# Performance work log

Measured on AMD Instinct MI355X. Metric: run time of the kernel, lower is better.

The kernel has to match this reference:

```python
import jax, jax.numpy as jnp
import numpy as np
import math

B, S, D, H = 4, 1024, 1024, 16
HD = D // H  # 64
DFF = 4 * D
LN_EPS = 1e-5

def setup_inputs() -> dict:
    key = jax.random.key(0)
    ks = jax.random.split(key, 24)
    sd = lambda fi, fo: 1.0 / math.sqrt(fi)
    def lin(k, fi, fo):
        k1, k2 = jax.random.split(k)
        w = jax.random.uniform(k1, (fi, fo), jnp.float32, -sd(fi, fo), sd(fi, fo))
        b = jax.random.uniform(k2, (fo,), jnp.float32, -sd(fi, fo), sd(fi, fo))
        return w, b
    x = jax.random.normal(ks[0], (B, S, D), jnp.float32)
    Wk, bk = lin(ks[1], D, D)
    Wq, bq = lin(ks[2], D, D)
    Wv, bv = lin(ks[3], D, D)
    # per-head projections stacked over heads: [H, D, HD]
    def head_lin(k):
        kk = jax.random.split(k, H)
        ws, bs = zip(*[lin(kk[h], D, HD) for h in range(H)])
        return jnp.stack(ws), jnp.stack(bs)
    Whq, bhq = head_lin(ks[4])
    Whk, bhk = head_lin(ks[5])
    Whv, bhv = head_lin(ks[6])
    Wo, bo = lin(ks[7], D, D)
    W1, b1 = lin(ks[8], D, DFF)
    W2, b2 = lin(ks[9], DFF, D)
    gamma = jnp.ones((D,), jnp.float32)
    beta = jnp.zeros((D,), jnp.float32)
    return dict(x=x, Wk=Wk, bk=bk, Wq=Wq, bq=bq, Wv=Wv, bv=bv,
                Whq=Whq, bhq=bhq, Whk=Whk, bhk=bhk, Whv=Whv, bhv=bhv,
                Wo=Wo, bo=bo, W1=W1, b1=b1, W2=W2, b2=b2,
                gamma=gamma, beta=beta)

def _layer_norm(x, gamma, beta):
    mu = jnp.mean(x, axis=-1, keepdims=True)
    var = jnp.mean(jnp.square(x - mu), axis=-1, keepdims=True)
    return (x - mu) * jax.lax.rsqrt(var + LN_EPS) * gamma + beta

def reference(x, Wk, bk, Wq, bq, Wv, bv, Whq, bhq, Whk, bhk, Whv, bhv,
              Wo, bo, W1, b1, W2, b2, gamma, beta):
    # outer projections; NOTE: forward passes (k, q, v) into MHA, so the
    # MHA 'Q' stream is k_proj(x), 'K' stream is q_proj(x), 'V' is v_proj(x)
    ko = x @ Wk + bk
    qo = x @ Wq + bq
    vo = x @ Wv + bv
    # per-head projections (batched over heads): [B,H,S,HD]
    q = jnp.einsum('bsd,hde->bhse', ko, Whq) + bhq[None, :, None, :]
    k = jnp.einsum('bsd,hde->bhse', qo, Whk) + bhk[None, :, None, :]
    v = jnp.einsum('bsd,hde->bhse', vo, Whv) + bhv[None, :, None, :]
    # NOTE: original scales by sqrt(d_model), not sqrt(head_dim)
    scores = jnp.einsum('bhse,bhte->bhst', q, k) / math.sqrt(D)
    w = jax.nn.softmax(scores, axis=-1)
    o = jnp.einsum('bhst,bhte->bhse', w, v)         # [B,H,S,HD]
    o = o.transpose(0, 2, 1, 3).reshape(B, S, D)    # concat heads
    attn = o @ Wo + bo
    # dropout is identity in eval; shared LayerNorm after both residuals
    r1 = _layer_norm(x + attn, gamma, beta)
    ff = jax.nn.gelu(r1 @ W1 + b1, approximate=False) @ W2 + b2
    out = _layer_norm(r1 + ff, gamma, beta)
    return out
```

## Files before the change

### kernel.cpp

```cpp
#include <hip/hip_runtime.h>
#include <cstdint>
#include <cstddef>

#define D_MODEL 1024
#define SEQ 1024
#define BATCH 4
#define NHEAD 16
#define HDIM 64
#define ROWS (BATCH*SEQ)

typedef unsigned short u16;
typedef __attribute__((ext_vector_type(4))) unsigned short u16x4;
typedef __attribute__((ext_vector_type(8))) unsigned short u16x8;
typedef __attribute__((ext_vector_type(8))) __bf16 bf16x8v;
typedef __attribute__((ext_vector_type(4))) float f32x4;

__device__ inline u16 f2bf(float f){
  union{float f; unsigned u;} c; c.f = f;
  unsigned r = c.u + 0x7FFFu + ((c.u>>16)&1u);
  return (u16)(r>>16);
}
__device__ inline float bf2f(u16 s){
  union{unsigned u; float f;} c; c.u = ((unsigned)s)<<16; return c.f;
}
__device__ inline float gelu_f(float x){ return 0.5f*x*(1.f+erff(x*0.7071067811865475f)); }

__device__ __forceinline__ void gload_lds16(const void* g, void* l){
  __builtin_amdgcn_global_load_lds(
    (const __attribute__((address_space(1))) unsigned int*)g,
    (__attribute__((address_space(3))) unsigned int*)l, 16, 0, 0);
}

__global__ __launch_bounds__(256) void convert_bf(const float* __restrict__ in, u16* __restrict__ out){
  size_t idx = (size_t)blockIdx.x*256 + threadIdx.x;
  f32x4 v = *(const f32x4*)(in + idx*4);
  u16x4 o = { f2bf(v.x), f2bf(v.y), f2bf(v.z), f2bf(v.w) };
  *(u16x4*)(out + idx*4) = o;
}

struct C3 { const float* src[3]; u16* dst[3]; };
__global__ __launch_bounds__(256) void convert_w3(C3 p){
  int z = blockIdx.z;
  size_t idx = (size_t)blockIdx.x*256 + threadIdx.x;
  f32x4 v = *(const f32x4*)(p.src[z] + idx*4);
  u16x4 o = { f2bf(v.x), f2bf(v.y), f2bf(v.z), f2bf(v.w) };
  *(u16x4*)(p.dst[z] + idx*4) = o;
}

__global__ __launch_bounds__(256) void transpose_conv(const float* __restrict__ W, u16* __restrict__ WT, int K, int N){
  __shared__ float tile[32][33];
  int n0 = blockIdx.x*32, k0 = blockIdx.y*32;
  int tx = threadIdx.x & 31, ty = threadIdx.x >> 5;
  #pragma unroll
  for (int i=0;i<4;i++){
    int r = ty + i*8;
    tile[r][tx] = W[(size_t)(k0+r)*N + n0 + tx];
  }
  __syncthreads();
  #pragma unroll
  for (int i=0;i<4;i++){
    int r = ty + i*8;
    WT[(size_t)(n0+r)*K + k0 + tx] = f2bf(tile[tx][r]);
  }
}

struct H3 { const float* src[3]; u16* dst[3]; };
__global__ __launch_bounds__(256) void head_transpose3(H3 p){
  __shared__ float tile[32][33];
  int z = blockIdx.z; int which = z >> 4; int h = z & 15;
  const float* Wh = p.src[which];
  u16* WT = p.dst[which];
  int d0 = blockIdx.x*32, e0 = blockIdx.y*32;
  int tx = threadIdx.x & 31, ty = threadIdx.x >> 5;
  #pragma unroll
  for (int i=0;i<4;i++){
    int r = ty + i*8;
    tile[r][tx] = Wh[(size_t)h*D_MODEL*HDIM + (size_t)(d0+r)*HDIM + e0 + tx];
  }
  __syncthreads();
  #pragma unroll
  for (int i=0;i<4;i++){
    int r = ty + i*8;
    WT[(size_t)(h*HDIM + e0 + r)*D_MODEL + d0 + tx] = f2bf(tile[tx][r]);
  }
}

__global__ __launch_bounds__(64) void bias_comb(
  const float* bk, const float* bq, const float* bv,
  const float* Whq, const float* Whk, const float* Whv,
  const float* bhq, const float* bhk, const float* bhv, float* bc)
{
  int blk = blockIdx.x; int which = blk >> 4; int h = blk & 15; int e = threadIdx.x;
  const float* bvec = (which==0) ? bk : (which==1) ? bq : bv;
  const float* Wh   = (which==0) ? Whq : (which==1) ? Whk : Whv;
  const float* bh   = (which==0) ? bhq : (which==1) ? bhk : bhv;
  float s = bh[h*HDIM + e];
  const float* w = Wh + (size_t)h*D_MODEL*HDIM + e;
  for (int d=0; d<D_MODEL; ++d) s += bvec[d] * w[(size_t)d*HDIM];
  bc[which*1024 + h*HDIM + e] = s;
}

__global__ __launch_bounds__(512,2) void gemm256_8p(
  const u16* __restrict__ A, const u16* __restrict__ BT, const float* __restrict__ bias,
  u16* __restrict__ outB, int N, int K, int mode, int act)
{
  __shared__ __align__(16) u16 As[2][2][128*64];
  __shared__ __align__(16) u16 Bs[2][2][128*64];
  int t = threadIdx.x, lane = t&63, wid = t>>6;
  int wr = wid>>2, wc = wid&3;
  int fr = lane&15, kg = lane>>4;
  int gx = gridDim.x;
  int bid = blockIdx.y*gx + blockIdx.x;
  int nwg = gx*gridDim.y;
  int cpx = nwg>>3;
  int sw = (bid&7)*cpx + (bid>>3);
  int tc = sw % gx, tr = sw / gx;

  const u16* Abase = A  + (size_t)tr*256*K;
  const u16* Bbase = BT + (size_t)tc*256*K;
  int srow = lane>>3, sch8 = lane&7;

  f32x4 acc[8][4];
  #pragma unroll
  for (int m=0;m<8;m++)
    #pragma unroll
    for (int n=0;n<4;n++) acc[m][n] = (f32x4)0.f;

  bf16x8v af[2][4], bv0[2][2], bv1[2][2];

  #define STAGE_A8(buf,h,kt) { _Pragma("unroll") for (int li=0;li<2;li++){ \
    int sr = (wid*2+li)*8 + srow; \
    int gr = ((sr>>6)<<7) + (h)*64 + (sr&63); \
    int sc = sch8 ^ (sr&7); \
    gload_lds16(Abase + (size_t)gr*K + (size_t)(kt)*64 + sc*8, &As[buf][h][(wid*2+li)*512]); } }
  #define STAGE_B8(buf,h,kt) { _Pragma("unroll") for (int li=0;li<2;li++){ \
    int sr = (wid*2+li)*8 + srow; \
    int gc = ((sr>>5)<<6) + (h)*32 + (sr&31); \
    int sc = sch8 ^ (sr&7); \
    gload_lds16(Bbase + (size_t)gc*K + (size_t)(kt)*64 + sc*8, &Bs[buf][h][(wid*2+li)*512]); } }
  #define LDA8(buf,h) { _Pragma("unroll") for (int ks=0;ks<2;ks++) _Pragma("unroll") for (int mf=0;mf<4;mf++){ \
    int r = wr*64 + mf*16 + fr; \
    af[ks][mf] = *(const bf16x8v*)&As[buf][h][r*64 + (((kg+4*ks)^(r&7)))*8]; } }
  #define LDB8(buf,h,dst) { _Pragma("unroll") for (int ks=0;ks<2;ks++) _Pragma("unroll") for (int nf=0;nf<2;nf++){ \
    int r = wc*32 + nf*16 + fr; \
    dst[ks][nf] = *(const bf16x8v*)&Bs[buf][h][r*64 + (((kg+4*ks)^(r&7)))*8]; } }
  #define MM8(mq,nq,bv) { asm volatile("s_waitcnt lgkmcnt(0)" ::: "memory"); \
    __builtin_amdgcn_s_setprio(1); \
    _Pragma("unroll") for (int ks=0;ks<2;ks++) _Pragma("unroll") for (int mf=0;mf<4;mf++) _Pragma("unroll") for (int nf=0;nf<2;nf++) \
      acc[(mq)*4+mf][(nq)*2+nf] = __builtin_amdgcn_mfma_f32_16x16x32_bf16(af[ks][mf], bv[ks][nf], acc[(mq)*4+mf][(nq)*2+nf], 0,0,0); \
    __builtin_amdgcn_s_setprio(0); }
  #define BAR asm volatile("s_barrier" ::: "memory")

  int NT = K >> 6;
  STAGE_A8(0,0,0); STAGE_B8(0,0,0); STAGE_B8(0,1,0); STAGE_A8(0,1,0);
  asm volatile("s_waitcnt vmcnt(4)" ::: "memory");
  BAR;

  for (int kt=0; kt<NT; ++kt){
    int buf = kt&1, nb = buf^1;
    int pre = (kt+1 < NT);
    LDA8(buf,0); LDB8(buf,0,bv0);
    if (pre){ STAGE_A8(nb,0,kt+1); asm volatile("s_waitcnt vmcnt(4)" ::: "memory"); }
    else    {                      asm volatile("s_waitcnt vmcnt(2)" ::: "memory"); }
    BAR; MM8(0,0,bv0); BAR;
    LDB8(buf,1,bv1);
    if (pre){ STAGE_B8(nb,0,kt+1); asm volatile("s_waitcnt vmcnt(4)" ::: "memory"); }
    else    {                      asm volatile("s_waitcnt vmcnt(0)" ::: "memory"); }
    BAR; MM8(0,1,bv1); BAR;
    LDA8(buf,1);
    if (pre){ STAGE_B8(nb,1,kt+1); asm volatile("s_waitcnt vmcnt(6)" ::: "memory"); }
    BAR; MM8(1,1,bv1); BAR;
    if (pre){ STAGE_A8(nb,1,kt+1); asm volatile("s_waitcnt vmcnt(4)" ::: "memory"); }
    BAR; MM8(1,0,bv0); BAR;
  }

  int crow0 = tr*256 + wr*128;
  int ccol0 = tc*256 + wc*64;
  #pragma unroll
  for (int n=0;n<4;n++){
    int col = ccol0 + n*16 + fr;
    float bv = bias[col];
    #pragma unroll
    for (int m=0;m<8;m++){
      int rbase = crow0 + m*16 + kg*4;
      #pragma unroll
      for (int i=0;i<4;i++){
        float v = acc[m][n][i] + bv;
        if (act) v = gelu_f(v);
        int row = rbase + i;
        if (mode == 1){
          outB[(size_t)row*N + col] = f2bf(v);
        } else {
          int panel = col >> 10, c1 = col & 1023;
          if (panel < 2)
            outB[(size_t)panel*((size_t)ROWS*1024) + (size_t)row*1024 + c1] = f2bf(v);
          else {
            int b = row >> 10, s = row & 1023;
            int hh = c1 >> 6, e = c1 & 63;
            outB[(size_t)2*((size_t)ROWS*1024) + (((size_t)((b*NHEAD+hh)*HDIM+e))<<10) + s] = f2bf(v);
          }
        }
      }
    }
  }
}

__device__ __forceinline__ void stage128(u16 (*As)[4096], u16 (*Bs)[4096], int b,
  const u16* Ab, const u16* Bb, int Kstride, int kt, int wid, int rr, int sch)
{
  #pragma unroll
  for (int c=0;c<2;c++){
    int reg = c*4 + wid;
    int row = reg*16 + rr;
    gload_lds16(Ab + (size_t)row*Kstride + kt*32 + sch*8, &As[b][reg*512]);
  }
  #pragma unroll
  for (int c=0;c<2;c++){
    int reg = c*4 + wid;
    int row = reg*16 + rr;
    gload_lds16(Bb + (size_t)row*Kstride + kt*32 + sch*8, &Bs[b][reg*512]);
  }
}

__device__ __forceinline__ void gemm128_core(u16 (*As)[4096], u16 (*Bs)[4096],
  const u16* __restrict__ A, const u16* __restrict__ BT, const float* __restrict__ bias,
  float* __restrict__ outF, u16* __restrict__ outB,
  int N, int Kstride, int kofs, int Ksub, int mode, int act, int addbias)
{
  int t = threadIdx.x, lane = t&63, wid = t>>6;
  int wr = wid>>1, wc = wid&1;
  int fr = lane&15, kg = lane>>4;
  int gx = gridDim.x;
  int bid = blockIdx.y*gx + blockIdx.x;
  int nwg = gx*gridDim.y;
  int cpx = nwg >> 3;
  int sw = (bid&7)*cpx + (bid>>3);
  int tc = sw % gx, tr = sw / gx;

  const u16* Ab = A  + (size_t)tr*128*Kstride + kofs;
  const u16* Bb = BT + (size_t)tc*128*Kstride + kofs;
  int rr = lane>>2, cc = lane&3;
  int sch = cc ^ ((rr>>1)&3);

  f32x4 acc[4][4];
  #pragma unroll
  for (int m=0;m<4;m++)
    #pragma unroll
    for (int n=0;n<4;n++) acc[m][n] = (f32x4)0.f;

  int NT = Ksub >> 5;

  stage128(As, Bs, 0, Ab, Bb, Kstride, 0, wid, rr, sch);
  stage128(As, Bs, 1, Ab, Bb, Kstride, 1, wid, rr, sch);
  int buf = 0;
  for (int kt=0; kt<NT; ++kt){
    if (kt+2 < NT){
      int nb = buf+2; if (nb>=3) nb-=3;
      stage128(As, Bs, nb, Ab, Bb, Kstride, kt+2, wid, rr, sch);
      asm volatile("s_waitcnt vmcnt(8)" ::: "memory");
    } else if (kt+1 < NT){
      asm volatile("s_waitcnt vmcnt(4)" ::: "memory");
    } else {
      asm volatile("s_waitcnt vmcnt(0)" ::: "memory");
    }
    asm volatile("s_barrier" ::: "memory");
    bf16x8v af[4], bfv[4];
    #pragma unroll
    for (int m=0;m<4;m++){
      int r = wr*64 + m*16 + fr;
      af[m] = *(const bf16x8v*)&As[buf][r*32 + (kg ^ ((r>>1)&3))*8];
    }
    #pragma unroll
    for (int n=0;n<4;n++){
      int r = wc*64 + n*16 + fr;
      bfv[n] = *(const bf16x8v*)&Bs[buf][r*32 + (kg ^ ((r>>1)&3))*8];
    }
    #pragma unroll
    for (int m=0;m<4;m++)
      #pragma unroll
      for (int n=0;n<4;n++)
        acc[m][n] = __builtin_amdgcn_mfma_f32_16x16x32_bf16(af[m], bfv[n], acc[m][n], 0,0,0);
    if (kt+1 < NT)
      asm volatile("s_barrier" ::: "memory");
    buf += 1; if (buf >= 3) buf = 0;
  }

  int crow0 = tr*128 + wr*64;
  int ccol0 = tc*128 + wc*64;
  #pragma unroll
  for (int n=0;n<4;n++){
    int col = ccol0 + n*16 + fr;
    float bv = addbias ? bias[col] : 0.f;
    #pragma unroll
    for (int m=0;m<4;m++){
      int rbase = crow0 + m*16 + kg*4;
      #pragma unroll
      for (int i=0;i<4;i++){
        float v = acc[m][n][i] + bv;
        if (act) v = gelu_f(v);
        int row = rbase + i;
        if (mode == 1){
          outB[(size_t)row*N + col] = f2bf(v);
        } else {
          outF[(size_t)row*1024 + col] = v;
        }
      }
    }
  }
}

__global__ __launch_bounds__(256) void g_gemm_sk(
  const u16* A, const u16* BT, const float* bias, float* outBase, int K)
{
  __shared__ __align__(16) u16 As[3][4096];
  __shared__ __align__(16) u16 Bs[3][4096];
  int z = blockIdx.z;
  int Ksub = K >> 1;
  gemm128_core(As, Bs, A, BT, bias, outBase + (size_t)z*ROWS*1024, nullptr,
               1024, K, z*Ksub, Ksub, 3, 0, z==0);
}

struct B3 { const u16* A[3]; const u16* BT[3]; u16* Cb[3]; };
__global__ __launch_bounds__(256) void g_gemm_b3(B3 p, const float* bias){
  __shared__ __align__(16) u16 As[3][4096];
  __shared__ __align__(16) u16 Bs[3][4096];
  int z = blockIdx.z;
  gemm128_core(As, Bs, p.A[z], p.BT[z], bias, nullptr, p.Cb[z],
               1024, 1024, 0, 1024, 1, 0, 0);
}

__global__ __launch_bounds__(256) void attn_mfma(const u16* __restrict__ Q, const u16* __restrict__ Km,
                                                 const u16* __restrict__ Vt, u16* __restrict__ O)
{
  __shared__ __align__(16) u16 Ks[2][64*64];
  __shared__ __align__(16) u16 Vs[2][64*64];
  __shared__ __align__(16) u16 Ps[4][16*64];
  int t = threadIdx.x, lane = t & 63, wid = t >> 6;
  int fr = lane & 15, kg = lane >> 4;
  int qt = blockIdx.x, h = blockIdx.y, b = blockIdx.z;
  const size_t qkbase = ((size_t)b*SEQ)*D_MODEL + (size_t)h*HDIM;
  const size_t vtb = ((size_t)(b*NHEAD + h))*HDIM*SEQ;

  int qrow = qt*64 + wid*16 + fr;
  bf16x8v aq0 = *(const bf16x8v*)(Q + qkbase + (size_t)qrow*D_MODEL + kg*8);
  bf16x8v aq1 = *(const bf16x8v*)(Q + qkbase + (size_t)qrow*D_MODEL + 32 + kg*8);

  f32x4 Oacc[4];
  #pragma unroll
  for (int n=0;n<4;n++) Oacc[n] = (f32x4)0.f;
  float m_run[4], l_run[4];
  #pragma unroll
  for (int i=0;i<4;i++){ m_run[i] = -3e38f; l_run[i] = 0.f; }

  int srow = lane >> 3;
  int sch  = (lane & 7) ^ srow;
  int x7 = fr & 7;
  const float CS = 0.03125f * 1.4426950408889634f;
  u16* Pw = &Ps[wid][0];

  #define ASTG(bf,kt) { _Pragma("unroll") for (int c=0;c<2;c++){ \
    int r0 = (wid*2 + c)*8; int rowk = r0 + srow; \
    gload_lds16(Km + qkbase + (size_t)((kt)*64 + rowk)*D_MODEL + sch*8, &Ks[bf][r0*64]); \
    gload_lds16(Vt + vtb + (size_t)rowk*SEQ + (kt)*64 + sch*8, &Vs[bf][r0*64]); } }

  ASTG(0,0);
  asm volatile("s_waitcnt vmcnt(0)" ::: "memory");
  __syncthreads();

  for (int kt = 0; kt < SEQ/64; ++kt){
    int bf = kt & 1;
    if (kt+1 < SEQ/64) ASTG(bf^1, kt+1);

    f32x4 s4[4];
    #pragma unroll
    for (int n=0;n<4;n++){
      int r = n*16 + fr;
      bf16x8v k0 = *(const bf16x8v*)&Ks[bf][r*64 + ((kg  ) ^ x7)*8];
      bf16x8v k1 = *(const bf16x8v*)&Ks[bf][r*64 + ((4+kg) ^ x7)*8];
      f32x4 z = (f32x4)0.f;
      z = __builtin_amdgcn_mfma_f32_16x16x32_bf16(aq0, k0, z, 0,0,0);
      s4[n] = __builtin_amdgcn_mfma_f32_16x16x32_bf16(aq1, k1, z, 0,0,0);
    }
    #pragma unroll
    for (int n=0;n<4;n++) s4[n] *= CS;

    float mI[4];
    #pragma unroll
    for (int i=0;i<4;i++)
      mI[i] = fmaxf(fmaxf(s4[0][i], s4[1][i]), fmaxf(s4[2][i], s4[3][i]));
    #pragma unroll
    for (int off=1; off<16; off<<=1){
      #pragma unroll
      for (int i=0;i<4;i++) mI[i] = fmaxf(mI[i], __shfl_xor(mI[i], off));
    }
    float g = -3e38f;
    #pragma unroll
    for (int i=0;i<4;i++) g = fmaxf(g, mI[i] - m_run[i]);
    if (__any(g > 8.f)){
      #pragma unroll
      for (int i=0;i<4;i++){
        float mn = fmaxf(m_run[i], mI[i]);
        float sc = exp2f(m_run[i] - mn);
        m_run[i] = mn;
        l_run[i] *= sc;
        #pragma unroll
        for (int n=0;n<4;n++) Oacc[n][i] *= sc;
      }
    }
    float ls[4] = {0.f,0.f,0.f,0.f};
    #pragma unroll
    for (int n=0;n<4;n++){
      int chunk = n*2 + (fr>>3);
      #pragma unroll
      for (int i=0;i<4;i++){
        float pv = exp2f(s4[n][i] - m_run[i]);
        ls[i] += pv;
        int row = kg*4 + i;
        Pw[row*64 + (chunk ^ (row&7))*8 + (fr&7)] = f2bf(pv);
      }
    }
    #pragma unroll
    for (int off=1; off<16; off<<=1){
      #pragma unroll
      for (int i=0;i<4;i++) ls[i] += __shfl_xor(ls[i], off);
    }
    #pragma unroll
    for (int i=0;i<4;i++) l_run[i] += ls[i];
    asm volatile("s_waitcnt lgkmcnt(0)" ::: "memory");

    bf16x8v ap0 = *(const bf16x8v*)&Pw[fr*64 + ((kg  ) ^ x7)*8];
    bf16x8v ap1 = *(const bf16x8v*)&Pw[fr*64 + ((4+kg) ^ x7)*8];
    #pragma unroll
    for (int n2=0;n2<4;n2++){
      int r = n2*16 + fr;
      bf16x8v v0 = *(const bf16x8v*)&Vs[bf][r*64 + ((kg  ) ^ x7)*8];
      bf16x8v v1 = *(const bf16x8v*)&Vs[bf][r*64 + ((4+kg) ^ x7)*8];
      Oacc[n2] = __builtin_amdgcn_mfma_f32_16x16x32_bf16(ap0, v0, Oacc[n2], 0,0,0);
      Oacc[n2] = __builtin_amdgcn_mfma_f32_16x16x32_bf16(ap1, v1, Oacc[n2], 0,0,0);
    }
    asm volatile("s_waitcnt vmcnt(0)" ::: "memory");
    __syncthreads();
  }

  float inv[4];
  #pragma unroll
  for (int i=0;i<4;i++) inv[i] = 1.f / l_run[i];
  #pragma unroll
  for (int n2=0;n2<4;n2++){
    #pragma unroll
    for (int i=0;i<4;i++){
      int row = qt*64 + wid*16 + kg*4 + i;
      O[qkbase + (size_t)row*D_MODEL + n2*16 + fr] = f2bf(Oacc[n2][i]*inv[i]);
    }
  }
}

__global__ __launch_bounds__(256) void ln_sum3(const float* __restrict__ A, const float* __restrict__ B,
   const float* __restrict__ C, const float* __restrict__ gamma, const float* __restrict__ beta,
   float* __restrict__ Of, u16* __restrict__ Ob)
{
  int row = blockIdx.x, t = threadIdx.x;
  size_t base = (size_t)row*D_MODEL + t*4;
  f32x4 v = *(const f32x4*)(A + base);
  v += *(const f32x4*)(B + base);
  v += *(const f32x4*)(C + base);
  float s = v.x+v.y+v.z+v.w;
  float q = v.x*v.x+v.y*v.y+v.z*v.z+v.w*v.w;
  #pragma unroll
  for (int off=1; off<64; off<<=1){ s += __shfl_xor(s,off); q += __shfl_xor(q,off); }
  __shared__ float red[8];
  int wid = t>>6;
  if ((t&63)==0){ red[wid] = s; red[wid+4] = q; }
  __syncthreads();
  s = red[0]+red[1]+red[2]+red[3];
  q = red[4]+red[5]+red[6]+red[7];
  float mu = s*(1.f/1024.f);
  float var = q*(1.f/1024.f) - mu*mu;
  float rs = rsqrtf(var + 1e-5f);
  f32x4 g4 = *(const f32x4*)(gamma + t*4);
  f32x4 b4 = *(const f32x4*)(beta + t*4);
  f32x4 o;
  o.x = (v.x-mu)*rs*g4.x + b4.x;
  o.y = (v.y-mu)*rs*g4.y + b4.y;
  o.z = (v.z-mu)*rs*g4.z + b4.z;
  o.w = (v.w-mu)*rs*g4.w + b4.w;
  if (Of) *(f32x4*)(Of + base) = o;
  if (Ob){
    u16x4 ob = { f2bf(o.x), f2bf(o.y), f2bf(o.z), f2bf(o.w) };
    *(u16x4*)(Ob + base) = ob;
  }
}

extern "C" void kernel_launch(void* const* d_in, const int* in_sizes, int n_in,
                              void* d_out, int out_size, void* d_ws, size_t ws_size,
                              hipStream_t stream)
{
  const float* x    = (const float*)d_in[0];
  const float* Wk   = (const float*)d_in[1];
  const float* bk   = (const float*)d_in[2];
  const float* Wq   = (const float*)d_in[3];
  const float* bq   = (const float*)d_in[4];
  const float* Wv   = (const float*)d_in[5];
  const float* bv   = (const float*)d_in[6];
  const float* Whq  = (const float*)d_in[7];
  const float* bhq  = (const float*)d_in[8];
  const float* Whk  = (const float*)d_in[9];
  const float* bhk  = (const float*)d_in[10];
  const float* Whv  = (const float*)d_in[11];
  const float* bhv  = (const float*)d_in[12];
  const float* Wo   = (const float*)d_in[13];
  const float* bo   = (const float*)d_in[14];
  const float* W1   = (const float*)d_in[15];
  const float* b1   = (const float*)d_in[16];
  const float* W2   = (const float*)d_in[17];
  const float* b2   = (const float*)d_in[18];
  const float* gamma= (const float*)d_in[19];
  const float* beta = (const float*)d_in[20];

  char* ws = (char*)d_ws;
  const size_t MB_ = 1024*1024;
  u16* Wkb  = (u16*)(ws + 0*MB_);
  u16* Wqb  = (u16*)(ws + 2*MB_);
  u16* Wvb  = (u16*)(ws + 4*MB_);
  u16* WhqT = (u16*)(ws + 6*MB_);
  u16* WhkT = (u16*)(ws + 8*MB_);
  u16* WhvT = (u16*)(ws + 10*MB_);
  u16* WoT  = (u16*)(ws + 12*MB_);
  u16* W1T  = (u16*)(ws + 14*MB_);
  u16* W2T  = (u16*)(ws + 22*MB_);
  u16* xb   = (u16*)(ws + 30*MB_);
  u16* WcT  = (u16*)(ws + 38*MB_);
  float* bc = (float*)(ws + 44*MB_);
  u16* qb   = (u16*)(ws + 46*MB_);
  u16* kb   = (u16*)(ws + 54*MB_);
  u16* vt   = (u16*)(ws + 62*MB_);
  u16* Ob   = (u16*)(ws + 70*MB_);
  float* Pa = (float*)(ws + 78*MB_);
  float* Pb = (float*)(ws + 94*MB_);
  float* r1f = (float*)(ws + 110*MB_);
  u16*  r1b  = (u16*)(ws + 38*MB_);
  u16*  ff1b = (u16*)(ws + 46*MB_);

  dim3 tb(256);

  convert_bf<<<dim3(ROWS*D_MODEL/4/256), tb, 0, stream>>>(x, xb);
  C3 cw; cw.src[0]=Wk; cw.src[1]=Wq; cw.src[2]=Wv;
  cw.dst[0]=Wkb; cw.dst[1]=Wqb; cw.dst[2]=Wvb;
  convert_w3<<<dim3(1024,1,3), tb, 0, stream>>>(cw);
  H3 hh; hh.src[0]=Whq; hh.src[1]=Whk; hh.src[2]=Whv;
  hh.dst[0]=WhqT; hh.dst[1]=WhkT; hh.dst[2]=WhvT;
  head_transpose3<<<dim3(32,2,48), tb, 0, stream>>>(hh);
  transpose_conv<<<dim3(32,32),  tb, 0, stream>>>(Wo, WoT, 1024, 1024);
  transpose_conv<<<dim3(128,32), tb, 0, stream>>>(W1, W1T, 1024, 4096);
  transpose_conv<<<dim3(32,128), tb, 0, stream>>>(W2, W2T, 4096, 1024);
  bias_comb<<<dim3(48), dim3(64), 0, stream>>>(bk,bq,bv, Whq,Whk,Whv, bhq,bhk,bhv, bc);

  B3 cmb;
  cmb.A[0]=WhqT; cmb.A[1]=WhkT; cmb.A[2]=WhvT;
  cmb.BT[0]=Wkb; cmb.BT[1]=Wqb; cmb.BT[2]=Wvb;
  cmb.Cb[0]=WcT; cmb.Cb[1]=WcT+1048576; cmb.Cb[2]=WcT+2097152;
  g_gemm_b3<<<dim3(8,8,3), tb, 0, stream>>>(cmb, bk);

  gemm256_8p<<<dim3(12,16), dim3(512), 0, stream>>>(xb, WcT, bc, qb, 3072, 1024, 2, 0);

  attn_mfma<<<dim3(16,16,4), tb, 0, stream>>>(qb, kb, vt, Ob);

  g_gemm_sk<<<dim3(8,32,2), tb, 0, stream>>>(Ob, WoT, bo, Pa, 1024);
  ln_sum3<<<dim3(4096), tb, 0, stream>>>(x, Pa, Pb, gamma, beta, r1f, r1b);
  gemm256_8p<<<dim3(16,16), dim3(512), 0, stream>>>(r1b, W1T, b1, ff1b, 4096, 1024, 1, 1);
  g_gemm_sk<<<dim3(8,32,2), tb, 0, stream>>>(ff1b, W2T, b2, Pa, 4096);
  ln_sum3<<<dim3(4096), tb, 0, stream>>>(r1f, Pa, Pb, gamma, beta, (float*)d_out, nullptr);

  (void)in_sizes; (void)n_in; (void)out_size; (void)ws_size;
}
```

Measured before the change: 355.8 us.

## Merge conversion launches, simplify GEMM pipeline, single-buffer attention K/V

Merges the x/weight bf16 conversions into one launch and the three weight transposes into one launch to cut launch overhead. The 256x256 GEMM drops its fine-grained interleaved staging and barriers in favour of staging the whole next tile up front with one barrier per k-step, and its launch bounds drop to one block per SM. The attention kernel switches from double-buffered to single-buffered K/V, loading and waiting each tile before compute. This saves LDS and barriers, but it gives up overlap of the K/V loads with compute.

```diff
diff --git a/kernel.cpp b/kernel.cpp
--- a/kernel.cpp
+++ b/kernel.cpp
@@ -31,25 +31,29 @@
     (__attribute__((address_space(3))) unsigned int*)l, 16, 0, 0);
 }
 
-__global__ __launch_bounds__(256) void convert_bf(const float* __restrict__ in, u16* __restrict__ out){
-  size_t idx = (size_t)blockIdx.x*256 + threadIdx.x;
-  f32x4 v = *(const f32x4*)(in + idx*4);
+struct C4 { const float* src[4]; u16* dst[4]; };
+__global__ __launch_bounds__(256) void convert4(C4 p){
+  int bid = blockIdx.x;
+  int which, off;
+  if (bid < 4096){ which = 0; off = bid; }
+  else { which = 1 + ((bid-4096) >> 10); off = (bid-4096) & 1023; }
+  size_t idx = (size_t)off*256 + threadIdx.x;
+  f32x4 v = *(const f32x4*)(p.src[which] + idx*4);
   u16x4 o = { f2bf(v.x), f2bf(v.y), f2bf(v.z), f2bf(v.w) };
-  *(u16x4*)(out + idx*4) = o;
-}
-
-struct C3 { const float* src[3]; u16* dst[3]; };
-__global__ __launch_bounds__(256) void convert_w3(C3 p){
-  int z = blockIdx.z;
-  size_t idx = (size_t)blockIdx.x*256 + threadIdx.x;
-  f32x4 v = *(const f32x4*)(p.src[z] + idx*4);
-  u16x4 o = { f2bf(v.x), f2bf(v.y), f2bf(v.z), f2bf(v.w) };
-  *(u16x4*)(p.dst[z] + idx*4) = o;
-}
-
-__global__ __launch_bounds__(256) void transpose_conv(const float* __restrict__ W, u16* __restrict__ WT, int K, int N){
+  *(u16x4*)(p.dst[which] + idx*4) = o;
+}
+
+struct T3 { const float* W[3]; u16* WT[3]; };
+__global__ __launch_bounds__(256) void transpose3(T3 p){
   __shared__ float tile[32][33];
-  int n0 = blockIdx.x*32, k0 = blockIdx.y*32;
+  int bid = blockIdx.x;
+  int which, bx, by, K, N;
+  if (bid < 1024){ which=0; K=1024; N=1024; bx=bid&31;  by=bid>>5; }
+  else if (bid < 5120){ int i=bid-1024; which=1; K=1024; N=4096; bx=i&127; by=i>>7; }
+  else { int i=bid-5120; which=2; K=4096; N=1024; bx=i&31; by=i>>5; }
+  const float* W = p.W[which];
+  u16* WT = p.WT[which];
+  int n0 = bx*32, k0 = by*32;
   int tx = threadIdx.x & 31, ty = threadIdx.x >> 5;
   #pragma unroll
   for (int i=0;i<4;i++){
@@ -100,7 +104,7 @@
   bc[which*1024 + h*HDIM + e] = s;
 }
 
-__global__ __launch_bounds__(512,2) void gemm256_8p(
+__global__ __launch_bounds__(512,1) void gemm256_8p(
   const u16* __restrict__ A, const u16* __restrict__ BT, const float* __restrict__ bias,
   u16* __restrict__ outB, int N, int K, int mode, int act)
 {
@@ -138,6 +142,7 @@
     int gc = ((sr>>5)<<6) + (h)*32 + (sr&31); \
     int sc = sch8 ^ (sr&7); \
     gload_lds16(Bbase + (size_t)gc*K + (size_t)(kt)*64 + sc*8, &Bs[buf][h][(wid*2+li)*512]); } }
+  #define STAGE_ALL(buf,kt) { STAGE_A8(buf,0,kt); STAGE_B8(buf,0,kt); STAGE_B8(buf,1,kt); STAGE_A8(buf,1,kt); }
   #define LDA8(buf,h) { _Pragma("unroll") for (int ks=0;ks<2;ks++) _Pragma("unroll") for (int mf=0;mf<4;mf++){ \
     int r = wr*64 + mf*16 + fr; \
     af[ks][mf] = *(const bf16x8v*)&As[buf][h][r*64 + (((kg+4*ks)^(r&7)))*8]; } }
@@ -152,26 +157,21 @@
   #define BAR asm volatile("s_barrier" ::: "memory")
 
   int NT = K >> 6;
-  STAGE_A8(0,0,0); STAGE_B8(0,0,0); STAGE_B8(0,1,0); STAGE_A8(0,1,0);
-  asm volatile("s_waitcnt vmcnt(4)" ::: "memory");
-  BAR;
+  STAGE_ALL(0,0);
 
   for (int kt=0; kt<NT; ++kt){
     int buf = kt&1, nb = buf^1;
-    int pre = (kt+1 < NT);
-    LDA8(buf,0); LDB8(buf,0,bv0);
-    if (pre){ STAGE_A8(nb,0,kt+1); asm volatile("s_waitcnt vmcnt(4)" ::: "memory"); }
-    else    {                      asm volatile("s_waitcnt vmcnt(2)" ::: "memory"); }
-    BAR; MM8(0,0,bv0); BAR;
-    LDB8(buf,1,bv1);
-    if (pre){ STAGE_B8(nb,0,kt+1); asm volatile("s_waitcnt vmcnt(4)" ::: "memory"); }
-    else    {                      asm volatile("s_waitcnt vmcnt(0)" ::: "memory"); }
-    BAR; MM8(0,1,bv1); BAR;
-    LDA8(buf,1);
-    if (pre){ STAGE_B8(nb,1,kt+1); asm volatile("s_waitcnt vmcnt(6)" ::: "memory"); }
-    BAR; MM8(1,1,bv1); BAR;
-    if (pre){ STAGE_A8(nb,1,kt+1); asm volatile("s_waitcnt vmcnt(4)" ::: "memory"); }
-    BAR; MM8(1,0,bv0); BAR;
+    if (kt+1 < NT){
+      STAGE_ALL(nb, kt+1);
+      asm volatile("s_waitcnt vmcnt(8)" ::: "memory");
+    } else {
+      asm volatile("s_waitcnt vmcnt(0)" ::: "memory");
+    }
+    BAR;
+    LDA8(buf,0); LDB8(buf,0,bv0); MM8(0,0,bv0);
+    LDB8(buf,1,bv1);              MM8(0,1,bv1);
+    LDA8(buf,1);                  MM8(1,1,bv1);
+                                  MM8(1,0,bv0);
   }
 
   int crow0 = tr*256 + wr*128;
@@ -332,8 +332,8 @@
 __global__ __launch_bounds__(256) void attn_mfma(const u16* __restrict__ Q, const u16* __restrict__ Km,
                                                  const u16* __restrict__ Vt, u16* __restrict__ O)
 {
-  __shared__ __align__(16) u16 Ks[2][64*64];
-  __shared__ __align__(16) u16 Vs[2][64*64];
+  __shared__ __align__(16) u16 Ks[64*64];
+  __shared__ __align__(16) u16 Vs[64*64];
   __shared__ __align__(16) u16 Ps[4][16*64];
   int t = threadIdx.x, lane = t & 63, wid = t >> 6;
   int fr = lane & 15, kg = lane >> 4;
@@ -358,25 +358,24 @@
   const float CS = 0.03125f * 1.4426950408889634f;
   u16* Pw = &Ps[wid][0];
 
-  #define ASTG(bf,kt) { _Pragma("unroll") for (int c=0;c<2;c++){ \
-    int r0 = (wid*2 + c)*8; int rowk = r0 + srow; \
-    gload_lds16(Km + qkbase + (size_t)((kt)*64 + rowk)*D_MODEL + sch*8, &Ks[bf][r0*64]); \
-    gload_lds16(Vt + vtb + (size_t)rowk*SEQ + (kt)*64 + sch*8, &Vs[bf][r0*64]); } }
-
-  ASTG(0,0);
-  asm volatile("s_waitcnt vmcnt(0)" ::: "memory");
-  __syncthreads();
-
   for (int kt = 0; kt < SEQ/64; ++kt){
-    int bf = kt & 1;
-    if (kt+1 < SEQ/64) ASTG(bf^1, kt+1);
+    __syncthreads();
+    #pragma unroll
+    for (int c=0;c<2;c++){
+      int r0 = (wid*2 + c)*8;
+      int rowk = r0 + srow;
+      gload_lds16(Km + qkbase + (size_t)(kt*64 + rowk)*D_MODEL + sch*8, &Ks[r0*64]);
+      gload_lds16(Vt + vtb + (size_t)rowk*SEQ + kt*64 + sch*8, &Vs[r0*64]);
+    }
+    asm volatile("s_waitcnt vmcnt(0)" ::: "memory");
+    __syncthreads();
 
     f32x4 s4[4];
     #pragma unroll
     for (int n=0;n<4;n++){
       int r = n*16 + fr;
-      bf16x8v k0 = *(const bf16x8v*)&Ks[bf][r*64 + ((kg  ) ^ x7)*8];
-      bf16x8v k1 = *(const bf16x8v*)&Ks[bf][r*64 + ((4+kg) ^ x7)*8];
+      bf16x8v k0 = *(const bf16x8v*)&Ks[r*64 + ((kg  ) ^ x7)*8];
+      bf16x8v k1 = *(const bf16x8v*)&Ks[r*64 + ((4+kg) ^ x7)*8];
       f32x4 z = (f32x4)0.f;
       z = __builtin_amdgcn_mfma_f32_16x16x32_bf16(aq0, k0, z, 0,0,0);
       s4[n] = __builtin_amdgcn_mfma_f32_16x16x32_bf16(aq1, k1, z, 0,0,0);
@@ -433,13 +432,11 @@
     #pragma unroll
     for (int n2=0;n2<4;n2++){
       int r = n2*16 + fr;
-      bf16x8v v0 = *(const bf16x8v*)&Vs[bf][r*64 + ((kg  ) ^ x7)*8];
-      bf16x8v v1 = *(const bf16x8v*)&Vs[bf][r*64 + ((4+kg) ^ x7)*8];
+      bf16x8v v0 = *(const bf16x8v*)&Vs[r*64 + ((kg  ) ^ x7)*8];
+      bf16x8v v1 = *(const bf16x8v*)&Vs[r*64 + ((4+kg) ^ x7)*8];
       Oacc[n2] = __builtin_amdgcn_mfma_f32_16x16x32_bf16(ap0, v0, Oacc[n2], 0,0,0);
       Oacc[n2] = __builtin_amdgcn_mfma_f32_16x16x32_bf16(ap1, v1, Oacc[n2], 0,0,0);
     }
-    asm volatile("s_waitcnt vmcnt(0)" ::: "memory");
-    __syncthreads();
   }
 
   float inv[4];
@@ -543,16 +540,15 @@
 
   dim3 tb(256);
 
-  convert_bf<<<dim3(ROWS*D_MODEL/4/256), tb, 0, stream>>>(x, xb);
-  C3 cw; cw.src[0]=Wk; cw.src[1]=Wq; cw.src[2]=Wv;
-  cw.dst[0]=Wkb; cw.dst[1]=Wqb; cw.dst[2]=Wvb;
-  convert_w3<<<dim3(1024,1,3), tb, 0, stream>>>(cw);
+  C4 cv; cv.src[0]=x; cv.src[1]=Wk; cv.src[2]=Wq; cv.src[3]=Wv;
+  cv.dst[0]=xb; cv.dst[1]=Wkb; cv.dst[2]=Wqb; cv.dst[3]=Wvb;
+  convert4<<<dim3(4096+3072), tb, 0, stream>>>(cv);
   H3 hh; hh.src[0]=Whq; hh.src[1]=Whk; hh.src[2]=Whv;
   hh.dst[0]=WhqT; hh.dst[1]=WhkT; hh.dst[2]=WhvT;
   head_transpose3<<<dim3(32,2,48), tb, 0, stream>>>(hh);
-  transpose_conv<<<dim3(32,32),  tb, 0, stream>>>(Wo, WoT, 1024, 1024);
-  transpose_conv<<<dim3(128,32), tb, 0, stream>>>(W1, W1T, 1024, 4096);
-  transpose_conv<<<dim3(32,128), tb, 0, stream>>>(W2, W2T, 4096, 1024);
+  T3 tt; tt.W[0]=Wo; tt.W[1]=W1; tt.W[2]=W2;
+  tt.WT[0]=WoT; tt.WT[1]=W1T; tt.WT[2]=W2T;
+  transpose3<<<dim3(9216), tb, 0, stream>>>(tt);
   bias_comb<<<dim3(48), dim3(64), 0, stream>>>(bk,bq,bv, Whq,Whk,Whv, bhq,bhk,bhv, bc);
 
   B3 cmb;
```

Result: faster. 333.0 us (-6.4%).
